# Performance work log

Hardware: AMD Instinct MI355X
Metric: run time of the kernel (lower is better)

## Reference

```python
import jax, jax.numpy as jnp
import numpy as np

D_MODEL = 1024
N_HEADS = 16
D_K = D_MODEL // N_HEADS
D_FF = 4096
THETA = 10000.0
B, S = 2, 2048
EPS = 1e-5


def _trunc_normal(key, shape, fan_in, fan_out):
    std = np.sqrt(2.0 / (fan_in + fan_out))
    return std * jax.random.truncated_normal(key, -3.0, 3.0, shape, dtype=jnp.float32)


def setup_inputs() -> dict:
    key = jax.random.key(0)
    ks = jax.random.split(key, 9)
    x = jax.random.normal(ks[0], (B, S, D_MODEL), dtype=jnp.float32)
    wq = _trunc_normal(ks[1], (D_MODEL, D_MODEL), D_MODEL, D_MODEL)
    wk = _trunc_normal(ks[2], (D_MODEL, D_MODEL), D_MODEL, D_MODEL)
    wv = _trunc_normal(ks[3], (D_MODEL, D_MODEL), D_MODEL, D_MODEL)
    wo = _trunc_normal(ks[4], (D_MODEL, D_MODEL), D_MODEL, D_MODEL)
    w1 = _trunc_normal(ks[5], (D_FF, D_MODEL), D_MODEL, D_FF)
    w2 = _trunc_normal(ks[6], (D_MODEL, D_FF), D_FF, D_MODEL)
    w3 = _trunc_normal(ks[7], (D_FF, D_MODEL), D_MODEL, D_FF)
    g1 = jnp.ones((D_MODEL,), dtype=jnp.float32)
    g2 = jnp.ones((D_MODEL,), dtype=jnp.float32)
    return {"x": x, "wq": wq, "wk": wk, "wv": wv, "wo": wo,
            "w1": w1, "w2": w2, "w3": w3, "g1": g1, "g2": g2}


def _rmsnorm(x, gain):
    xf = x.astype(jnp.float32)
    rms = jnp.sqrt(jnp.mean(xf * xf, axis=-1, keepdims=True) + EPS)
    return (xf / rms * gain).astype(x.dtype)


def _rope(x):
    # x: [B, H, S, D_K]; block-diag 2x2 rotations on consecutive pairs
    s, d = x.shape[-2], x.shape[-1]
    pos = jnp.arange(s, dtype=jnp.float32)  # [S]
    k = jnp.arange(d // 2, dtype=jnp.float32)
    ang = pos[:, None] / (THETA ** (2.0 * k / d))[None, :]  # [S, d/2]
    cos, sin = jnp.cos(ang), jnp.sin(ang)
    xp = x.reshape(*x.shape[:-1], d // 2, 2)
    x0, x1 = xp[..., 0], xp[..., 1]
    r0 = cos * x0 - sin * x1
    r1 = sin * x0 + cos * x1
    return jnp.stack([r0, r1], axis=-1).reshape(x.shape)


def reference(x, wq, wk, wv, wo, w1, w2, w3, g1, g2):
    # --- attention sublayer ---
    h = _rmsnorm(x, g1)
    q = h @ wq.T
    k = h @ wk.T
    v = h @ wv.T
    def split_heads(t):
        b, s, _ = t.shape
        return t.reshape(b, s, N_HEADS, D_K).transpose(0, 2, 1, 3)  # [B,H,S,Dk]
    q, k, v = split_heads(q), split_heads(k), split_heads(v)
    q, k = _rope(q), _rope(k)
    scores = jnp.einsum('bhqd,bhkd->bhqk', q, k) / jnp.sqrt(jnp.float32(D_K))
    s = x.shape[-2]
    causal = jnp.tril(jnp.ones((s, s), dtype=bool))
    scores = jnp.where(causal, scores, -jnp.inf)
    attn = jax.nn.softmax(scores, axis=-1)
    o = jnp.einsum('bhqk,bhkd->bhqd', attn, v)
    o = o.transpose(0, 2, 1, 3).reshape(x.shape[0], s, D_MODEL)
    x = x + o @ wo.T
    # --- SwiGLU FFN sublayer ---
    h2 = _rmsnorm(x, g2)
    a = h2 @ w1.T
    gate = a * jax.nn.sigmoid(a)
    ff = (gate * (h2 @ w3.T)) @ w2.T
    return x + ff
```

## Files before the change

kernel.cpp:

```cpp
#include <hip/hip_runtime.h>
#include <hip/hip_bf16.h>
#include <cstddef>
#include <cstdint>

#define D_MODEL 1024
#define N_HEADS 16
#define D_K     64
#define D_FF    4096
#define BATCH   2
#define SEQ     2048
#define TOKENS  (BATCH * SEQ)
#define EPS     1e-5f

typedef __attribute__((ext_vector_type(8))) short short8;
typedef __attribute__((ext_vector_type(4))) float f32x4;

#define MFMA_BF16 __builtin_amdgcn_mfma_f32_16x16x32_bf16

static __device__ __forceinline__ short f2bf(float f) {
    __hip_bfloat16 h = __float2bfloat16(f);
    short s;
    __builtin_memcpy(&s, &h, 2);
    return s;
}
static __device__ __forceinline__ float bf2f(short s) {
    __hip_bfloat16 h;
    __builtin_memcpy(&h, &s, 2);
    return __bfloat162float(h);
}

static __device__ __forceinline__ void async_ld16(const short* g, short* l) {
    __builtin_amdgcn_global_load_lds(
        (const __attribute__((address_space(1))) void*)g,
        (__attribute__((address_space(3))) void*)l,
        16, 0, 0);
}

__global__ __launch_bounds__(256) void cvt_weights(
    const float* wq, const float* wk, const float* wv, const float* wo,
    const float* w1, const float* w3, const float* w2, short* dst)
{
    const size_t M1 = 1 << 20;
    size_t e = ((size_t)blockIdx.x * 256 + threadIdx.x) * 4;
    const float* src;
    size_t off;
    if (e < M1)            { src = wq; off = e; }
    else if (e < 2 * M1)   { src = wk; off = e - M1; }
    else if (e < 3 * M1)   { src = wv; off = e - 2 * M1; }
    else if (e < 4 * M1)   { src = wo; off = e - 3 * M1; }
    else if (e < 12 * M1) {
        size_t r = (e - 4 * M1) >> 10;
        size_t col = e & 1023;
        size_t p = r >> 5, half = (r >> 4) & 1, idx = r & 15;
        src = half ? w3 : w1;
        off = (p * 16 + idx) * 1024 + col;
    }
    else                   { src = w2; off = e - 12 * M1; }
    float4 v = *reinterpret_cast<const float4*>(src + off);
    short4 o;
    o.x = f2bf(v.x); o.y = f2bf(v.y); o.z = f2bf(v.z); o.w = f2bf(v.w);
    *reinterpret_cast<short4*>(dst + e) = o;
}

__global__ __launch_bounds__(256) void rmsnorm_kernel(
    const float* __restrict__ x, const float* __restrict__ g,
    __hip_bfloat16* __restrict__ out)
{
    int row = blockIdx.x;
    int tid = threadIdx.x;
    int lane = tid & 63, wave = tid >> 6;
    const float4* xv = reinterpret_cast<const float4*>(x + (size_t)row * D_MODEL);
    float4 v = xv[tid];
    float ss = v.x * v.x + v.y * v.y + v.z * v.z + v.w * v.w;
#pragma unroll
    for (int m = 1; m < 64; m <<= 1) ss += __shfl_xor(ss, m, 64);
    __shared__ float red[4];
    if (lane == 0) red[wave] = ss;
    __syncthreads();
    float tot = red[0] + red[1] + red[2] + red[3];
    float inv = 1.0f / sqrtf(tot * (1.0f / D_MODEL) + EPS);
    float4 gv = reinterpret_cast<const float4*>(g)[tid];
    size_t base = (size_t)row * D_MODEL + (size_t)tid * 4;
    out[base + 0] = __float2bfloat16(v.x * inv * gv.x);
    out[base + 1] = __float2bfloat16(v.y * inv * gv.y);
    out[base + 2] = __float2bfloat16(v.z * inv * gv.z);
    out[base + 3] = __float2bfloat16(v.w * inv * gv.w);
}

__global__ __launch_bounds__(256) void resid_norm_kernel(
    const float* __restrict__ x, const float* __restrict__ P,
    const float* __restrict__ g, float* __restrict__ out,
    __hip_bfloat16* __restrict__ h)
{
    int row = blockIdx.x;
    int tid = threadIdx.x;
    int lane = tid & 63, wave = tid >> 6;
    size_t base = (size_t)row * D_MODEL + (size_t)tid * 4;
    float4 v  = *reinterpret_cast<const float4*>(x + base);
    float4 p0 = *reinterpret_cast<const float4*>(P + base);
    float4 p1 = *reinterpret_cast<const float4*>(P + (size_t)TOKENS * D_MODEL + base);
    v.x += p0.x + p1.x; v.y += p0.y + p1.y;
    v.z += p0.z + p1.z; v.w += p0.w + p1.w;
    *reinterpret_cast<float4*>(out + base) = v;
    float ss = v.x * v.x + v.y * v.y + v.z * v.z + v.w * v.w;
#pragma unroll
    for (int m = 1; m < 64; m <<= 1) ss += __shfl_xor(ss, m, 64);
    __shared__ float red[4];
    if (lane == 0) red[wave] = ss;
    __syncthreads();
    float tot = red[0] + red[1] + red[2] + red[3];
    float inv = 1.0f / sqrtf(tot * (1.0f / D_MODEL) + EPS);
    float4 gv = reinterpret_cast<const float4*>(g)[tid];
    h[base + 0] = __float2bfloat16(v.x * inv * gv.x);
    h[base + 1] = __float2bfloat16(v.y * inv * gv.y);
    h[base + 2] = __float2bfloat16(v.z * inv * gv.z);
    h[base + 3] = __float2bfloat16(v.w * inv * gv.w);
}

__global__ __launch_bounds__(256) void final_add_kernel(
    float* __restrict__ out, const float* __restrict__ Q)
{
    size_t base = ((size_t)blockIdx.x * 256 + threadIdx.x) * 4;
    float4 v  = *reinterpret_cast<const float4*>(out + base);
    float4 q0 = *reinterpret_cast<const float4*>(Q + base);
    float4 q1 = *reinterpret_cast<const float4*>(Q + (size_t)TOKENS * D_MODEL + base);
    v.x += q0.x + q1.x; v.y += q0.y + q1.y;
    v.z += q0.z + q1.z; v.w += q0.w + q1.w;
    *reinterpret_cast<float4*>(out + base) = v;
}

template<int EPI>
__global__ __launch_bounds__(256) void gemm_bt(
    const short* __restrict__ A, const short* __restrict__ W,
    void* __restrict__ Cout, int K, int lda, int ldc)
{
    __shared__ short Alds[128 * 64];
    __shared__ short Blds[128 * 64];

    const int lane = threadIdx.x & 63;
    const int wv = threadIdx.x >> 6;
    const int quad = lane >> 4, l16 = lane & 15;
    const int wm = wv & 1, wn = wv >> 1;
    const int rowblk = blockIdx.y * 128;
    const int colblk = blockIdx.x * 128;

    const int srow = lane >> 2;
    const int sseg = ((lane & 3) - (lane >> 3)) & 3;
    const short* sA0 = A + (size_t)(rowblk + wv * 16 + srow) * lda + sseg * 8;
    const short* sA1 = A + (size_t)(rowblk + (wv + 4) * 16 + srow) * lda + sseg * 8;
    const short* sB0 = W + (size_t)(colblk + wv * 16 + srow) * (size_t)K + sseg * 8;
    const short* sB1 = W + (size_t)(colblk + (wv + 4) * 16 + srow) * (size_t)K + sseg * 8;
    short* lA0 = &Alds[wv * 512];
    short* lA1 = &Alds[(wv + 4) * 512];
    short* lB0 = &Blds[wv * 512];
    short* lB1 = &Blds[(wv + 4) * 512];

    int aoff[4], boff[4];
#pragma unroll
    for (int i = 0; i < 4; ++i) {
        int tr = wm * 64 + i * 16 + l16;
        aoff[i] = tr * 32 + ((quad + (tr >> 1)) & 3) * 8;
        int tc = wn * 64 + i * 16 + l16;
        boff[i] = tc * 32 + ((quad + (tc >> 1)) & 3) * 8;
    }

    f32x4 acc[4][4];
#pragma unroll
    for (int i = 0; i < 4; ++i)
#pragma unroll
        for (int j = 0; j < 4; ++j)
            acc[i][j] = (f32x4){0.f, 0.f, 0.f, 0.f};

    for (int kk = 0; kk < K; kk += 64) {
        if (kk) __syncthreads();
        async_ld16(sA0 + kk, lA0);
        async_ld16(sA1 + kk, lA1);
        async_ld16(sB0 + kk, lB0);
        async_ld16(sB1 + kk, lB1);
        async_ld16(sA0 + kk + 32, lA0 + 4096);
        async_ld16(sA1 + kk + 32, lA1 + 4096);
        async_ld16(sB0 + kk + 32, lB0 + 4096);
        async_ld16(sB1 + kk + 32, lB1 + 4096);
        __syncthreads();
#pragma unroll
        for (int hf = 0; hf < 2; ++hf) {
            short8 af[4], bf[4];
#pragma unroll
            for (int i = 0; i < 4; ++i)
                af[i] = *reinterpret_cast<const short8*>(&Alds[hf * 4096 + aoff[i]]);
#pragma unroll
            for (int j = 0; j < 4; ++j)
                bf[j] = *reinterpret_cast<const short8*>(&Blds[hf * 4096 + boff[j]]);
#pragma unroll
            for (int i = 0; i < 4; ++i)
#pragma unroll
                for (int j = 0; j < 4; ++j)
                    acc[i][j] = MFMA_BF16(af[i], bf[j], acc[i][j], 0, 0, 0);
        }
    }

    if (EPI == 2) {
#pragma unroll
        for (int i = 0; i < 4; ++i) {
#pragma unroll
            for (int jp = 0; jp < 2; ++jp) {
#pragma unroll
                for (int r = 0; r < 4; ++r) {
                    int row = rowblk + wm * 64 + i * 16 + quad * 4 + r;
                    int col = blockIdx.x * 64 + wn * 32 + jp * 16 + l16;
                    float a = acc[i][2 * jp][r];
                    float b3 = acc[i][2 * jp + 1][r];
                    float gv = a / (1.f + __expf(-a)) * b3;
                    reinterpret_cast<__hip_bfloat16*>(Cout)[(size_t)row * ldc + col] =
                        __float2bfloat16(gv);
                }
            }
        }
    } else {
#pragma unroll
        for (int i = 0; i < 4; ++i) {
#pragma unroll
            for (int j = 0; j < 4; ++j) {
#pragma unroll
                for (int r = 0; r < 4; ++r) {
                    int row = rowblk + wm * 64 + i * 16 + quad * 4 + r;
                    int col = colblk + wn * 64 + j * 16 + l16;
                    size_t idx = (size_t)row * ldc + col;
                    if (EPI == 3)
                        reinterpret_cast<__hip_bfloat16*>(Cout)[idx] =
                            __float2bfloat16(acc[i][j][r]);
                    else
                        reinterpret_cast<float*>(Cout)[idx] = acc[i][j][r];
                }
            }
        }
    }
}

template<int SPLIT>
__global__ __launch_bounds__(256) void gemm_bt_sk(
    const short* __restrict__ A, const short* __restrict__ W,
    float* __restrict__ P, int K, int lda, int ldc)
{
    __shared__ short Alds[128 * 64];
    __shared__ short Blds[128 * 64];

    const int Kc = K / SPLIT;
    const int kbase = blockIdx.z * Kc;
    float* Cout = P + (size_t)blockIdx.z * TOKENS * ldc;

    const int lane = threadIdx.x & 63;
    const int wv = threadIdx.x >> 6;
    const int quad = lane >> 4, l16 = lane & 15;
    const int wm = wv & 1, wn = wv >> 1;
    const int rowblk = blockIdx.y * 128;
    const int colblk = blockIdx.x * 128;

    const int srow = lane >> 2;
    const int sseg = ((lane & 3) - (lane >> 3)) & 3;
    const short* sA0 = A + (size_t)(rowblk + wv * 16 + srow) * lda + kbase + sseg * 8;
    const short* sA1 = A + (size_t)(rowblk + (wv + 4) * 16 + srow) * lda + kbase + sseg * 8;
    const short* sB0 = W + (size_t)(colblk + wv * 16 + srow) * (size_t)K + kbase + sseg * 8;
    const short* sB1 = W + (size_t)(colblk + (wv + 4) * 16 + srow) * (size_t)K + kbase + sseg * 8;
    short* lA0 = &Alds[wv * 512];
    short* lA1 = &Alds[(wv + 4) * 512];
    short* lB0 = &Blds[wv * 512];
    short* lB1 = &Blds[(wv + 4) * 512];

    int aoff[4], boff[4];
#pragma unroll
    for (int i = 0; i < 4; ++i) {
        int tr = wm * 64 + i * 16 + l16;
        aoff[i] = tr * 32 + ((quad + (tr >> 1)) & 3) * 8;
        int tc = wn * 64 + i * 16 + l16;
        boff[i] = tc * 32 + ((quad + (tc >> 1)) & 3) * 8;
    }

    f32x4 acc[4][4];
#pragma unroll
    for (int i = 0; i < 4; ++i)
#pragma unroll
        for (int j = 0; j < 4; ++j)
            acc[i][j] = (f32x4){0.f, 0.f, 0.f, 0.f};

    for (int kk = 0; kk < Kc; kk += 64) {
        if (kk) __syncthreads();
        async_ld16(sA0 + kk, lA0);
        async_ld16(sA1 + kk, lA1);
        async_ld16(sB0 + kk, lB0);
        async_ld16(sB1 + kk, lB1);
        async_ld16(sA0 + kk + 32, lA0 + 4096);
        async_ld16(sA1 + kk + 32, lA1 + 4096);
        async_ld16(sB0 + kk + 32, lB0 + 4096);
        async_ld16(sB1 + kk + 32, lB1 + 4096);
        __syncthreads();
#pragma unroll
        for (int hf = 0; hf < 2; ++hf) {
            short8 af[4], bf[4];
#pragma unroll
            for (int i = 0; i < 4; ++i)
                af[i] = *reinterpret_cast<const short8*>(&Alds[hf * 4096 + aoff[i]]);
#pragma unroll
            for (int j = 0; j < 4; ++j)
                bf[j] = *reinterpret_cast<const short8*>(&Blds[hf * 4096 + boff[j]]);
#pragma unroll
            for (int i = 0; i < 4; ++i)
#pragma unroll
                for (int j = 0; j < 4; ++j)
                    acc[i][j] = MFMA_BF16(af[i], bf[j], acc[i][j], 0, 0, 0);
        }
    }

#pragma unroll
    for (int i = 0; i < 4; ++i) {
#pragma unroll
        for (int j = 0; j < 4; ++j) {
#pragma unroll
            for (int r = 0; r < 4; ++r) {
                int row = rowblk + wm * 64 + i * 16 + quad * 4 + r;
                int col = colblk + wn * 64 + j * 16 + l16;
                Cout[(size_t)row * ldc + col] = acc[i][j][r];
            }
        }
    }
}

__global__ __launch_bounds__(256) void rope_kernel(
    const short* __restrict__ qk,
    __hip_bfloat16* __restrict__ qb, __hip_bfloat16* __restrict__ kb)
{
    int idx = blockIdx.x * 256 + threadIdx.x;
    int p = idx & 31;
    int h = (idx >> 5) & 15;
    int tok = idx >> 9;
    int s = tok & (SEQ - 1);
    int b = tok >> 11;
    float invf = exp2f((float)p * -(0.03125f * 13.287712379549449f));
    float ang = (float)s * invf;
    float c, sn;
    sincosf(ang, &sn, &c);
    size_t base = (size_t)tok * 3072 + h * 64 + 2 * p;
    float q0 = bf2f(qk[base]),           q1 = bf2f(qk[base + 1]);
    float k0 = bf2f(qk[base + D_MODEL]), k1 = bf2f(qk[base + D_MODEL + 1]);
    float cq = c * 0.125f, sq = sn * 0.125f;
    size_t ob = ((size_t)(b * N_HEADS + h) * SEQ + s) * D_K + 2 * p;
    qb[ob]     = __float2bfloat16(cq * q0 - sq * q1);
    qb[ob + 1] = __float2bfloat16(sq * q0 + cq * q1);
    kb[ob]     = __float2bfloat16(c * k0 - sn * k1);
    kb[ob + 1] = __float2bfloat16(sn * k0 + c * k1);
}

__global__ __launch_bounds__(256) void vtrans_kernel(
    const short* __restrict__ qk, __hip_bfloat16* __restrict__ vt)
{
    __shared__ float tile[64 * 65];
    const int bh = blockIdx.y;
    const int s0 = blockIdx.x * 64;
    const int t = threadIdx.x;
    const int r = t >> 4, c4 = (t & 15) * 4;
    const short* src = qk + ((size_t)(bh >> 4) * SEQ + s0) * 3072 + 2048 + (bh & 15) * 64;
#pragma unroll
    for (int p = 0; p < 4; ++p) {
        int s = p * 16 + r;
        short4 v = *reinterpret_cast<const short4*>(src + (size_t)s * 3072 + c4);
        tile[s * 65 + c4 + 0] = bf2f(v.x);
        tile[s * 65 + c4 + 1] = bf2f(v.y);
        tile[s * 65 + c4 + 2] = bf2f(v.z);
        tile[s * 65 + c4 + 3] = bf2f(v.w);
    }
    __syncthreads();
    const int d = t >> 2, sg = (t & 3) * 16;
    __hip_bfloat16* dst = vt + ((size_t)bh * 64 + d) * SEQ + s0 + sg;
    short8 o0, o1;
#pragma unroll
    for (int i = 0; i < 8; ++i) o0[i] = f2bf(tile[(sg + i) * 65 + d]);
#pragma unroll
    for (int i = 0; i < 8; ++i) o1[i] = f2bf(tile[(sg + 8 + i) * 65 + d]);
    *reinterpret_cast<short8*>(dst) = o0;
    *reinterpret_cast<short8*>(dst + 8) = o1;
}

__global__ __launch_bounds__(256) void attn_kernel(
    const __hip_bfloat16* __restrict__ qbp, const __hip_bfloat16* __restrict__ kbp,
    const __hip_bfloat16* __restrict__ vtp, __hip_bfloat16* __restrict__ o)
{
    const int wave = threadIdx.x >> 6;
    const int lane = threadIdx.x & 63;
    const int quad = lane >> 4, l16 = lane & 15;
    const int bh = blockIdx.y;
    const int t = blockIdx.x + wave * 16;
    const int q0 = t * 32;

    const short* Q  = reinterpret_cast<const short*>(qbp) + ((size_t)bh * SEQ + q0) * D_K;
    const short* Kp = reinterpret_cast<const short*>(kbp) + (size_t)bh * SEQ * D_K;
    const short* Vt = reinterpret_cast<const short*>(vtp) + (size_t)bh * D_K * SEQ;

    short8 qfr[2][2];
#pragma unroll
    for (int f = 0; f < 2; ++f) {
        qfr[f][0] = *reinterpret_cast<const short8*>(Q + (size_t)(f * 16 + l16) * D_K + quad * 8);
        qfr[f][1] = *reinterpret_cast<const short8*>(Q + (size_t)(f * 16 + l16) * D_K + 32 + quad * 8);
    }

    f32x4 oacc[2][4];
    f32x4 lacc[2];
#pragma unroll
    for (int f = 0; f < 2; ++f) {
        lacc[f] = (f32x4){0.f, 0.f, 0.f, 0.f};
#pragma unroll
        for (int g = 0; g < 4; ++g) oacc[f][g] = (f32x4){0.f, 0.f, 0.f, 0.f};
    }

    short8 ones;
#pragma unroll
    for (int i = 0; i < 8; ++i) ones[i] = (short)0x3F80;

    __shared__ short plds[4][32 * 36];
    short* myP = &plds[wave][0];

    for (int kk = 0; kk < q0 + 32; kk += 32) {
        f32x4 sf[2][2];
#pragma unroll
        for (int kg = 0; kg < 2; ++kg) {
            const short* Kr = Kp + (size_t)(kk + kg * 16 + l16) * D_K;
            short8 kf0 = *reinterpret_cast<const short8*>(Kr + quad * 8);
            short8 kf1 = *reinterpret_cast<const short8*>(Kr + 32 + quad * 8);
#pragma unroll
            for (int f = 0; f < 2; ++f) {
                f32x4 z = (f32x4){0.f, 0.f, 0.f, 0.f};
                z = MFMA_BF16(qfr[f][0], kf0, z, 0, 0, 0);
                z = MFMA_BF16(qfr[f][1], kf1, z, 0, 0, 0);
                sf[f][kg] = z;
            }
        }
#pragma unroll
        for (int f = 0; f < 2; ++f) {
            const int qlo = q0 + f * 16;
#pragma unroll
            for (int kg = 0; kg < 2; ++kg) {
                const int keylo = kk + kg * 16;
                const bool needmask = keylo >= qlo;
                const int key = keylo + l16;
#pragma unroll
                for (int r = 0; r < 4; ++r) {
                    float p = __expf(sf[f][kg][r]);
                    if (needmask) {
                        int qrow = qlo + quad * 4 + r;
                        p = (key > qrow) ? 0.f : p;
                    }
                    myP[(f * 16 + quad * 4 + r) * 36 + keylo - kk + l16] = f2bf(p);
                }
            }
        }
        asm volatile("s_waitcnt lgkmcnt(0)" ::: "memory");
        short8 pf[2];
#pragma unroll
        for (int f = 0; f < 2; ++f) {
            pf[f] = *reinterpret_cast<const short8*>(&myP[(f * 16 + l16) * 36 + quad * 8]);
            lacc[f] = MFMA_BF16(pf[f], ones, lacc[f], 0, 0, 0);
        }
#pragma unroll
        for (int g = 0; g < 4; ++g) {
            short8 vf = *reinterpret_cast<const short8*>(
                Vt + (size_t)(g * 16 + l16) * SEQ + kk + quad * 8);
#pragma unroll
            for (int f = 0; f < 2; ++f)
                oacc[f][g] = MFMA_BF16(pf[f], vf, oacc[f][g], 0, 0, 0);
        }
    }

    const int b = bh >> 4, h = bh & 15;
#pragma unroll
    for (int f = 0; f < 2; ++f) {
#pragma unroll
        for (int g = 0; g < 4; ++g) {
#pragma unroll
            for (int r = 0; r < 4; ++r) {
                int qrow = q0 + f * 16 + quad * 4 + r;
                float v = oacc[f][g][r] / lacc[f][r];
                o[(size_t)(b * SEQ + qrow) * D_MODEL + h * 64 + g * 16 + l16] =
                    __float2bfloat16(v);
            }
        }
    }
}

extern "C" void kernel_launch(void* const* d_in, const int* in_sizes, int n_in,
                              void* d_out, int out_size, void* d_ws, size_t ws_size,
                              hipStream_t stream)
{
    const float* x  = (const float*)d_in[0];
    const float* wq = (const float*)d_in[1];
    const float* wk = (const float*)d_in[2];
    const float* wv = (const float*)d_in[3];
    const float* wo = (const float*)d_in[4];
    const float* w1 = (const float*)d_in[5];
    const float* w2 = (const float*)d_in[6];
    const float* w3 = (const float*)d_in[7];
    const float* g1 = (const float*)d_in[8];
    const float* g2 = (const float*)d_in[9];
    float* out = (float*)d_out;

    char* ws = (char*)d_ws;
    const size_t OFF_WTS  = 0;
    const size_t OFF_H    = 33554432;
    const size_t OFF_QKV  = 41943040;
    const size_t OFF_QB   = 92274688;
    const size_t OFF_KB   = 100663296;
    const size_t OFF_VT   = 109051904;
    const size_t OFF_O    = 117440512;
    const size_t OFF_P    = OFF_QKV;
    const size_t OFF_GATE = OFF_QKV;
    const size_t OFF_Q2   = OFF_QB;

    short* wts  = (short*)(ws + OFF_WTS);
    short* wqkvb = wts;
    short* wob  = wts + (size_t)3 * (1 << 20);
    short* w13b = wts + (size_t)4 * (1 << 20);
    short* w2b  = wts + (size_t)12 * (1 << 20);
    __hip_bfloat16* h  = (__hip_bfloat16*)(ws + OFF_H);
    short* qkvb = (short*)(ws + OFF_QKV);
    __hip_bfloat16* qb = (__hip_bfloat16*)(ws + OFF_QB);
    __hip_bfloat16* kb = (__hip_bfloat16*)(ws + OFF_KB);
    __hip_bfloat16* vt = (__hip_bfloat16*)(ws + OFF_VT);
    __hip_bfloat16* ob = (__hip_bfloat16*)(ws + OFF_O);
    float* Pwo  = (float*)(ws + OFF_P);
    __hip_bfloat16* gate = (__hip_bfloat16*)(ws + OFF_GATE);
    float* Qw2  = (float*)(ws + OFF_Q2);

    cvt_weights<<<16384, 256, 0, stream>>>(wq, wk, wv, wo, w1, w3, w2, wts);
    rmsnorm_kernel<<<TOKENS, 256, 0, stream>>>(x, g1, h);
    gemm_bt<3><<<dim3(3072 / 128, TOKENS / 128), 256, 0, stream>>>(
        (const short*)h, wqkvb, qkvb, D_MODEL, D_MODEL, 3072);
    rope_kernel<<<8192, 256, 0, stream>>>(qkvb, qb, kb);
    vtrans_kernel<<<dim3(SEQ / 64, BATCH * N_HEADS), 256, 0, stream>>>(qkvb, vt);
    attn_kernel<<<dim3(16, BATCH * N_HEADS), 256, 0, stream>>>(qb, kb, vt, ob);
    gemm_bt_sk<2><<<dim3(D_MODEL / 128, TOKENS / 128, 2), 256, 0, stream>>>(
        (const short*)ob, wob, Pwo, D_MODEL, D_MODEL, D_MODEL);
    resid_norm_kernel<<<TOKENS, 256, 0, stream>>>(x, Pwo, g2, out, h);
    gemm_bt<2><<<dim3(8192 / 128, TOKENS / 128), 256, 0, stream>>>(
        (const short*)h, w13b, gate, D_MODEL, D_MODEL, D_FF);
    gemm_bt_sk<2><<<dim3(D_MODEL / 128, TOKENS / 128, 2), 256, 0, stream>>>(
        (const short*)gate, w2b, Qw2, D_FF, D_FF, D_MODEL);
    final_add_kernel<<<TOKENS * D_MODEL / 1024, 256, 0, stream>>>(out, Qw2);
    (void)in_sizes; (void)n_in; (void)out_size; (void)ws_size;
}
```

Baseline: 420.9 us.

## Stage K/V tiles in shared memory shared across waves in attention

Attention blocks now cover 128 contiguous query rows, with each wave taking 32 of them, instead of four interleaved 32-row tiles. Each 64-key K and V tile is loaded once per block into LDS using async loads and a rotated swizzle, then read by all four waves. Before, every wave read K and V straight from global memory. This cuts global and L2 traffic and gives larger MFMA steps per tile, but it adds block-wide barriers. The contiguous query split also gives blocks unequal causal work, which can hurt load balance.

```diff
diff --git a/kernel.cpp b/kernel.cpp
--- a/kernel.cpp
+++ b/kernel.cpp
@@ -388,12 +388,12 @@
     const int lane = threadIdx.x & 63;
     const int quad = lane >> 4, l16 = lane & 15;
     const int bh = blockIdx.y;
-    const int t = blockIdx.x + wave * 16;
-    const int q0 = t * 32;
+    const int qt = blockIdx.x;
+    const int q0 = qt * 128 + wave * 32;
 
     const short* Q  = reinterpret_cast<const short*>(qbp) + ((size_t)bh * SEQ + q0) * D_K;
-    const short* Kp = reinterpret_cast<const short*>(kbp) + (size_t)bh * SEQ * D_K;
-    const short* Vt = reinterpret_cast<const short*>(vtp) + (size_t)bh * D_K * SEQ;
+    const short* Kg = reinterpret_cast<const short*>(kbp) + (size_t)bh * SEQ * D_K;
+    const short* Vg = reinterpret_cast<const short*>(vtp) + (size_t)bh * D_K * SEQ;
 
     short8 qfr[2][2];
 #pragma unroll
@@ -415,16 +415,35 @@
 #pragma unroll
     for (int i = 0; i < 8; ++i) ones[i] = (short)0x3F80;
 
-    __shared__ short plds[4][32 * 36];
+    __shared__ short Kt[64 * 64];
+    __shared__ short Vl[64 * 64];
+    __shared__ short plds[4][32 * 72];
     short* myP = &plds[wave][0];
 
-    for (int kk = 0; kk < q0 + 32; kk += 32) {
-        f32x4 sf[2][2];
-#pragma unroll
-        for (int kg = 0; kg < 2; ++kg) {
-            const short* Kr = Kp + (size_t)(kk + kg * 16 + l16) * D_K;
-            short8 kf0 = *reinterpret_cast<const short8*>(Kr + quad * 8);
-            short8 kf1 = *reinterpret_cast<const short8*>(Kr + 32 + quad * 8);
+    const int srl = lane >> 3;
+    const int sp  = lane & 7;
+
+    const int ntile = 2 * qt + 2;
+    for (int tile = 0; tile < ntile; ++tile) {
+        const int kb0 = tile * 64;
+        if (tile) __syncthreads();
+#pragma unroll
+        for (int j = 0; j < 2; ++j) {
+            int r0 = j * 32 + wave * 8;
+            int t  = r0 + srl;
+            int sl = (sp - t) & 7;
+            async_ld16(Kg + (size_t)(kb0 + t) * D_K + sl * 8, &Kt[r0 * 64]);
+            async_ld16(Vg + (size_t)t * SEQ + kb0 + sl * 8, &Vl[r0 * 64]);
+        }
+        __syncthreads();
+
+        f32x4 sf[2][4];
+#pragma unroll
+        for (int kg = 0; kg < 4; ++kg) {
+            int row = kg * 16 + l16;
+            const short* kr = &Kt[row * 64];
+            short8 kf0 = *reinterpret_cast<const short8*>(&kr[((quad + row) & 7) * 8]);
+            short8 kf1 = *reinterpret_cast<const short8*>(&kr[((quad + 4 + row) & 7) * 8]);
 #pragma unroll
             for (int f = 0; f < 2; ++f) {
                 f32x4 z = (f32x4){0.f, 0.f, 0.f, 0.f};
@@ -437,8 +456,8 @@
         for (int f = 0; f < 2; ++f) {
             const int qlo = q0 + f * 16;
 #pragma unroll
-            for (int kg = 0; kg < 2; ++kg) {
-                const int keylo = kk + kg * 16;
+            for (int kg = 0; kg < 4; ++kg) {
+                const int keylo = kb0 + kg * 16;
                 const bool needmask = keylo >= qlo;
                 const int key = keylo + l16;
 #pragma unroll
@@ -448,24 +467,32 @@
                         int qrow = qlo + quad * 4 + r;
                         p = (key > qrow) ? 0.f : p;
                     }
-                    myP[(f * 16 + quad * 4 + r) * 36 + keylo - kk + l16] = f2bf(p);
+                    myP[(f * 16 + quad * 4 + r) * 72 + kg * 16 + l16] = f2bf(p);
                 }
             }
         }
         asm volatile("s_waitcnt lgkmcnt(0)" ::: "memory");
-        short8 pf[2];
+        short8 pf[2][2];
 #pragma unroll
         for (int f = 0; f < 2; ++f) {
-            pf[f] = *reinterpret_cast<const short8*>(&myP[(f * 16 + l16) * 36 + quad * 8]);
-            lacc[f] = MFMA_BF16(pf[f], ones, lacc[f], 0, 0, 0);
+#pragma unroll
+            for (int hh = 0; hh < 2; ++hh) {
+                pf[f][hh] = *reinterpret_cast<const short8*>(
+                    &myP[(f * 16 + l16) * 72 + (hh * 4 + quad) * 8]);
+                lacc[f] = MFMA_BF16(pf[f][hh], ones, lacc[f], 0, 0, 0);
+            }
         }
 #pragma unroll
         for (int g = 0; g < 4; ++g) {
-            short8 vf = *reinterpret_cast<const short8*>(
-                Vt + (size_t)(g * 16 + l16) * SEQ + kk + quad * 8);
-#pragma unroll
-            for (int f = 0; f < 2; ++f)
-                oacc[f][g] = MFMA_BF16(pf[f], vf, oacc[f][g], 0, 0, 0);
+            int rd = g * 16 + l16;
+            const short* vr = &Vl[rd * 64];
+            short8 vf0 = *reinterpret_cast<const short8*>(&vr[((quad + rd) & 7) * 8]);
+            short8 vf1 = *reinterpret_cast<const short8*>(&vr[((quad + 4 + rd) & 7) * 8]);
+#pragma unroll
+            for (int f = 0; f < 2; ++f) {
+                oacc[f][g] = MFMA_BF16(pf[f][0], vf0, oacc[f][g], 0, 0, 0);
+                oacc[f][g] = MFMA_BF16(pf[f][1], vf1, oacc[f][g], 0, 0, 0);
+            }
         }
     }
 
@@ -534,7 +561,7 @@
         (const short*)h, wqkvb, qkvb, D_MODEL, D_MODEL, 3072);
     rope_kernel<<<8192, 256, 0, stream>>>(qkvb, qb, kb);
     vtrans_kernel<<<dim3(SEQ / 64, BATCH * N_HEADS), 256, 0, stream>>>(qkvb, vt);
-    attn_kernel<<<dim3(16, BATCH * N_HEADS), 256, 0, stream>>>(qb, kb, vt, ob);
+    attn_kernel<<<dim3(SEQ / 128, BATCH * N_HEADS), 256, 0, stream>>>(qb, kb, vt, ob);
     gemm_bt_sk<2><<<dim3(D_MODEL / 128, TOKENS / 128, 2), 256, 0, stream>>>(
         (const short*)ob, wob, Pwo, D_MODEL, D_MODEL, D_MODEL);
     resid_norm_kernel<<<TOKENS, 256, 0, stream>>>(x, Pwo, g2, out, h);
```

New measurement: 399.3 us. -5.1%, faster.
